# Optimization experiments

Measured on AMD Instinct MI355X. Metric: run time of the kernel, lower is better.

Reference implementation:

```python
import jax, jax.numpy as jnp
import numpy as np
import math

DIM = 2048
NUM_HEADS = 16
NUM_KV_HEADS = 4
HEAD_DIM = DIM // NUM_HEADS  # 128
KV_DIM = DIM * NUM_KV_HEADS // NUM_HEADS  # 512
B, T = 4, 2048


def setup_inputs() -> dict:
    key = jax.random.key(0)
    ks = jax.random.split(key, 12)
    s = 0.02
    return {
        "x": jax.random.normal(ks[0], (B, T, DIM), dtype=jnp.float32),
        "cos": jax.random.uniform(ks[1], (T, HEAD_DIM // 2), dtype=jnp.float32),
        "sin": jax.random.uniform(ks[2], (T, HEAD_DIM // 2), dtype=jnp.float32),
        "Wq": jax.random.normal(ks[3], (DIM, DIM), dtype=jnp.float32) * s,
        "bq": jnp.zeros((DIM,), dtype=jnp.float32),
        "Wk": jax.random.normal(ks[4], (DIM, KV_DIM), dtype=jnp.float32) * s,
        "bk": jnp.zeros((KV_DIM,), dtype=jnp.float32),
        "Wv": jax.random.normal(ks[5], (DIM, KV_DIM), dtype=jnp.float32) * s,
        "bv": jnp.zeros((KV_DIM,), dtype=jnp.float32),
        "Wo": jax.random.normal(ks[6], (DIM, DIM), dtype=jnp.float32) * s,
        "bo": jnp.zeros((DIM,), dtype=jnp.float32),
    }


def _rope(t, cos, sin):
    # t: [B, H, T, D]; cos/sin: [T, D/2] broadcast over (B, H)
    t1, t2 = t[..., ::2], t[..., 1::2]
    return jnp.concatenate([t1 * cos - t2 * sin, t1 * sin + t2 * cos], axis=-1)


def reference(x, cos, sin, Wq, bq, Wk, bk, Wv, bv, Wo, bo):
    Bx, Tx, C = x.shape
    q = (x @ Wq + bq).reshape(Bx, Tx, NUM_HEADS, HEAD_DIM).transpose(0, 2, 1, 3)
    k = (x @ Wk + bk).reshape(Bx, Tx, NUM_KV_HEADS, HEAD_DIM).transpose(0, 2, 1, 3)
    v = (x @ Wv + bv).reshape(Bx, Tx, NUM_KV_HEADS, HEAD_DIM).transpose(0, 2, 1, 3)
    rep = NUM_HEADS // NUM_KV_HEADS
    k = jnp.repeat(k, rep, axis=1)
    v = jnp.repeat(v, rep, axis=1)
    q = _rope(q, cos, sin)
    k = _rope(k, cos, sin)
    scores = jnp.einsum("bhqd,bhkd->bhqk", q, k) / math.sqrt(HEAD_DIM)
    attn = jax.nn.softmax(scores, axis=-1)
    out = jnp.einsum("bhqk,bhkd->bhqd", attn, v)
    out = out.transpose(0, 2, 1, 3).reshape(Bx, Tx, C)
    return out @ Wo + bo
```

## Files before the change

### kernel.cpp

```cpp
#include <hip/hip_runtime.h>

typedef unsigned short u16;
using bf16x8 = __attribute__((ext_vector_type(8))) short;
using u16x8  = __attribute__((ext_vector_type(8))) unsigned short;
using f32x4  = __attribute__((ext_vector_type(4))) float;
using f32x16 = __attribute__((ext_vector_type(16))) float;
using u32x4  = __attribute__((ext_vector_type(4))) unsigned int;

__device__ __forceinline__ u16 f2bf(float f) {
  unsigned u = __float_as_uint(f);
  u += 0x7FFFu + ((u >> 16) & 1u);
  return (u16)(u >> 16);
}

__device__ __forceinline__ unsigned cvt_pk_bf16(float lo, float hi) {
  unsigned r;
  asm("v_cvt_pk_bf16_f32 %0, %1, %2" : "=v"(r) : "v"(lo), "v"(hi));
  return r;
}

__device__ __forceinline__ void permswap(unsigned& a, unsigned& b) {
  asm volatile("v_permlane32_swap_b32 %0, %1" : "+v"(a), "+v"(b));
}

__device__ __forceinline__ void gload_lds16(const void* g, void* l) {
  __builtin_amdgcn_global_load_lds(
      (const __attribute__((address_space(1))) unsigned int*)g,
      (__attribute__((address_space(3))) unsigned int*)l, 16, 0, 0);
}

__global__ __launch_bounds__(256) void k_cvt(const float* __restrict__ src,
                                             u16* __restrict__ dst) {
  size_t i = (size_t)blockIdx.x * 256 + threadIdx.x;
  const float4* s4 = (const float4*)src;
  float4 a = s4[i * 2], b = s4[i * 2 + 1];
  u16x8 r;
  r[0] = f2bf(a.x); r[1] = f2bf(a.y); r[2] = f2bf(a.z); r[3] = f2bf(a.w);
  r[4] = f2bf(b.x); r[5] = f2bf(b.y); r[6] = f2bf(b.z); r[7] = f2bf(b.w);
  *(u16x8*)(dst + i * 8) = r;
}

__global__ void k_transpose_cvt(const float* __restrict__ src, u16* __restrict__ dst,
                                int R, int C) {
  __shared__ float tile[32][33];
  int bx = blockIdx.x * 32, by = blockIdx.y * 32;
  int tx = threadIdx.x, ty = threadIdx.y;
#pragma unroll
  for (int j = 0; j < 4; ++j)
    tile[ty + j * 8][tx] = src[(size_t)(by + ty + j * 8) * C + bx + tx];
  __syncthreads();
#pragma unroll
  for (int j = 0; j < 4; ++j)
    dst[(size_t)(bx + ty + j * 8) * R + by + tx] = f2bf(tile[tx][ty + j * 8]);
}

__device__ __forceinline__ void gemm_core128(const u16* __restrict__ A,
                                             const u16* __restrict__ Bt, int K,
                                             int m0, int n0, u16* As, u16* Bs,
                                             f32x4 acc[4][4]) {
  const int tid  = threadIdx.x;
  const int lane = tid & 63;
  const int w    = tid >> 6;
  const int wr   = (w >> 1) * 64;
  const int wc   = (w & 1) * 64;
  const int srow = (w << 3) + (lane >> 3);
  const int lm   = lane & 15;
  const int lg   = lane >> 4;

  for (int kt = 0; kt < K; kt += 64) {
#pragma unroll
    for (int i = 0; i < 4; ++i) {
      int r  = (i << 5) + srow;
      int cc = (lane & 7) ^ (r & 7);
      gload_lds16(A  + (size_t)(m0 + r) * K + kt + (cc << 3), As + ((i * 4 + w) << 9));
      gload_lds16(Bt + (size_t)(n0 + r) * K + kt + (cc << 3), Bs + ((i * 4 + w) << 9));
    }
    __syncthreads();
#pragma unroll
    for (int kk = 0; kk < 2; ++kk) {
      bf16x8 af[4], bfr[4];
#pragma unroll
      for (int m = 0; m < 4; ++m) {
        const int row = wr + m * 16 + lm;
        af[m] = *(const bf16x8*)(As + row * 64 + ((((kk << 2) + lg) ^ (row & 7)) << 3));
      }
#pragma unroll
      for (int n = 0; n < 4; ++n) {
        const int row = wc + n * 16 + lm;
        bfr[n] = *(const bf16x8*)(Bs + row * 64 + ((((kk << 2) + lg) ^ (row & 7)) << 3));
      }
#pragma unroll
      for (int m = 0; m < 4; ++m)
#pragma unroll
        for (int n = 0; n < 4; ++n)
          acc[m][n] = __builtin_amdgcn_mfma_f32_16x16x32_bf16(af[m], bfr[n], acc[m][n], 0, 0, 0);
    }
    __syncthreads();
  }
}

__global__ __launch_bounds__(256, 2) void k_qkv(
    const u16* __restrict__ xb, const u16* __restrict__ wT,
    const float* __restrict__ bq, const float* __restrict__ bk, const float* __restrict__ bv,
    const float* __restrict__ cosb, const float* __restrict__ sinb,
    u16* __restrict__ qbuf, u16* __restrict__ kbuf, u16* __restrict__ vbufT) {
  __shared__ u16 As[128 * 64], Bs[128 * 64];
  const int mt = blockIdx.x, nt = blockIdx.y;
  f32x4 acc[4][4];
#pragma unroll
  for (int m = 0; m < 4; ++m)
#pragma unroll
    for (int n = 0; n < 4; ++n) { f32x4 z = {0.f, 0.f, 0.f, 0.f}; acc[m][n] = z; }
  gemm_core128(xb, wT, 2048, mt * 128, nt * 128, As, Bs, acc);

  const int lane = threadIdx.x & 63, w = threadIdx.x >> 6;
  const int row0 = mt * 128 + (w >> 1) * 64 + ((lane >> 4) << 2);
  const int col0 = nt * 128 + (w & 1) * 64 + (lane & 15);
  const float qscale = 0.12751744f;

#pragma unroll
  for (int m = 0; m < 4; ++m) {
#pragma unroll
    for (int n = 0; n < 4; ++n) {
      const int gc = col0 + n * 16;
#pragma unroll
      for (int i = 0; i < 4; ++i) {
        const int gr = row0 + m * 16 + i;
        const int b = gr >> 11, t = gr & 2047;
        float v = acc[m][n][i];
        if (nt < 16) {
          int h = gc >> 7, d = gc & 127;
          float val = v + bq[gc];
          float part = __shfl_xor(val, 1);
          int ir = d >> 1;
          float c = cosb[t * 64 + ir], s = sinb[t * 64 + ir];
          float outv; int dd;
          if (d & 1) { outv = part * s + val * c; dd = ir + 64; }
          else       { outv = val * c - part * s; dd = ir; }
          qbuf[(((size_t)(b * 16 + h) * 2048 + t) << 7) + dd] = f2bf(outv * qscale);
        } else if (nt < 20) {
          int g2 = gc - 2048;
          int kvh = g2 >> 7, d = g2 & 127;
          float val = v + bk[g2];
          float part = __shfl_xor(val, 1);
          int ir = d >> 1;
          float c = cosb[t * 64 + ir], s = sinb[t * 64 + ir];
          float outv; int dd;
          if (d & 1) { outv = part * s + val * c; dd = ir + 64; }
          else       { outv = val * c - part * s; dd = ir; }
          kbuf[(((size_t)(b * 4 + kvh) * 2048 + t) << 7) + dd] = f2bf(outv);
        } else {
          int g2 = gc - 2560;
          int kvh = g2 >> 7, d = g2 & 127;
          float val = v + bv[g2];
          vbufT[((size_t)((b * 4 + kvh) * 128 + d)) * 2048 + t] = f2bf(val);
        }
      }
    }
  }
}

__global__ __launch_bounds__(256, 2) void k_attn(const u16* __restrict__ qbuf,
                                                 const u16* __restrict__ kbuf,
                                                 const u16* __restrict__ vbufT,
                                                 u16* __restrict__ ob) {
  __shared__ u16 Ks[2][64 * 128];
  __shared__ u16 Vs[2][128 * 64];

  const int f = blockIdx.x;
  const int x = f & 7, mm = f >> 3;
  const int g = x * 2 + (mm >> 6);
  const int mem = mm & 63;
  const int b = g >> 2, kvh = g & 3;
  const int h = kvh * 4 + (mem >> 4);
  const int qt = mem & 15;

  const int tid = threadIdx.x, lane = tid & 63, w = tid >> 6;
  const int l31 = lane & 31, hi = lane >> 5;

  const u16* qb = qbuf + ((size_t)((b * 16 + h) * 2048 + qt * 128)) * 128;
  const u16* kb = kbuf + ((size_t)(b * 4 + kvh) * 2048) * 128;
  const u16* vb = vbufT + ((size_t)(b * 4 + kvh) * 128) * 2048;

  const int q = w * 32 + l31;
  bf16x8 qfr[8];
#pragma unroll
  for (int kc = 0; kc < 8; ++kc)
    qfr[kc] = *(const bf16x8*)(qb + (size_t)q * 128 + kc * 16 + hi * 8);

  f32x16 o[4];
#pragma unroll
  for (int dt = 0; dt < 4; ++dt)
#pragma unroll
    for (int r = 0; r < 16; ++r) o[dt][r] = 0.f;
  float lsum = 0.f;

  auto stage = [&](int buf, int kt) {
#pragma unroll
    for (int j = 0; j < 4; ++j) {
      int s  = w * 4 + j;
      int cK = s * 64 + lane;
      int rK = cK >> 4, ccK = cK & 15;
      gload_lds16(kb + (size_t)(kt + rK) * 128 + ((ccK ^ (rK & 7)) << 3), &Ks[buf][s << 9]);
      int dV = s * 8 + (lane >> 3), ccV = lane & 7;
      gload_lds16(vb + (size_t)dV * 2048 + kt + ((ccV ^ (dV & 7)) << 3), &Vs[buf][s << 9]);
    }
  };

  stage(0, 0);
  for (int t = 0; t < 32; ++t) {
    if (t < 31) {
      stage((t + 1) & 1, (t + 1) << 6);
      asm volatile("s_waitcnt vmcnt(8)" ::: "memory");
    } else {
      asm volatile("s_waitcnt vmcnt(0)" ::: "memory");
    }
    __builtin_amdgcn_s_barrier();
    __builtin_amdgcn_sched_barrier(0);
    const u16* KsC = Ks[t & 1];
    const u16* VsC = Vs[t & 1];

    u32x4 pa[4];

#pragma unroll
    for (int kb2 = 0; kb2 < 2; ++kb2) {
      const int key = kb2 * 32 + l31;
      bf16x8 kf[8];
#pragma unroll
      for (int kc = 0; kc < 8; ++kc)
        kf[kc] = *(const bf16x8*)(KsC + key * 128 + (((kc * 2 + hi) ^ (key & 7)) << 3));
      f32x16 s;
#pragma unroll
      for (int r = 0; r < 16; ++r) s[r] = 0.f;
      __builtin_amdgcn_s_setprio(1);
#pragma unroll
      for (int kc = 0; kc < 8; ++kc)
        s = __builtin_amdgcn_mfma_f32_32x32x16_bf16(kf[kc], qfr[kc], s, 0, 0, 0);
      __builtin_amdgcn_s_setprio(0);

      unsigned c[8];
#pragma unroll
      for (int j = 0; j < 8; ++j) {
        float pa_ = __builtin_amdgcn_exp2f(s[2 * j]);
        float pb_ = __builtin_amdgcn_exp2f(s[2 * j + 1]);
        lsum += pa_ + pb_;
        c[j] = cvt_pk_bf16(pa_, pb_);
      }
      unsigned t0 = c[0], t1 = c[2]; permswap(t0, t1);
      unsigned t2 = c[1], t3 = c[3]; permswap(t2, t3);
      u32x4 f0; f0[0] = t0; f0[1] = t2; f0[2] = t1; f0[3] = t3;
      pa[kb2 * 2] = f0;
      unsigned t4 = c[4], t5 = c[6]; permswap(t4, t5);
      unsigned t6 = c[5], t7 = c[7]; permswap(t6, t7);
      u32x4 f1; f1[0] = t4; f1[1] = t6; f1[2] = t5; f1[3] = t7;
      pa[kb2 * 2 + 1] = f1;
    }

    __builtin_amdgcn_s_setprio(1);
#pragma unroll
    for (int dt = 0; dt < 4; ++dt) {
      const int d = dt * 32 + l31;
#pragma unroll
      for (int ks = 0; ks < 4; ++ks) {
        bf16x8 vf = *(const bf16x8*)(VsC + d * 64 + (((ks * 2 + hi) ^ (d & 7)) << 3));
        bf16x8 af = __builtin_bit_cast(bf16x8, pa[ks]);
        o[dt] = __builtin_amdgcn_mfma_f32_32x32x16_bf16(af, vf, o[dt], 0, 0, 0);
      }
    }
    __builtin_amdgcn_s_setprio(0);
    __builtin_amdgcn_sched_barrier(0);
    __builtin_amdgcn_s_barrier();
  }

  float L = lsum + __shfl_xor(lsum, 32);
  float invL = 1.0f / L;
  float iv[16];
#pragma unroll
  for (int r = 0; r < 16; ++r)
    iv[r] = __shfl(invL, (r & 3) + 8 * (r >> 2) + 4 * hi);
#pragma unroll
  for (int dt = 0; dt < 4; ++dt) {
    const int d = dt * 32 + l31;
#pragma unroll
    for (int r = 0; r < 16; ++r) {
      const int tq = qt * 128 + w * 32 + (r & 3) + 8 * (r >> 2) + 4 * hi;
      ob[((size_t)(b * 2048 + tq)) * 2048 + h * 128 + d] = f2bf(o[dt][r] * iv[r]);
    }
  }
}

__global__ __launch_bounds__(256, 2) void k_oproj(const u16* __restrict__ ab,
                                                  const u16* __restrict__ woT,
                                                  const float* __restrict__ bo,
                                                  float* __restrict__ out) {
  __shared__ u16 As[128 * 64], Bs[128 * 64];
  const int mt = blockIdx.x, nt = blockIdx.y;
  f32x4 acc[4][4];
#pragma unroll
  for (int m = 0; m < 4; ++m)
#pragma unroll
    for (int n = 0; n < 4; ++n) { f32x4 z = {0.f, 0.f, 0.f, 0.f}; acc[m][n] = z; }
  gemm_core128(ab, woT, 2048, mt * 128, nt * 128, As, Bs, acc);

  const int lane = threadIdx.x & 63, w = threadIdx.x >> 6;
  const int row0 = mt * 128 + (w >> 1) * 64 + ((lane >> 4) << 2);
  const int col0 = nt * 128 + (w & 1) * 64 + (lane & 15);
#pragma unroll
  for (int m = 0; m < 4; ++m)
#pragma unroll
    for (int n = 0; n < 4; ++n) {
      const int gc = col0 + n * 16;
      const float bias = bo[gc];
#pragma unroll
      for (int i = 0; i < 4; ++i) {
        const int gr = row0 + m * 16 + i;
        out[(size_t)gr * 2048 + gc] = acc[m][n][i] + bias;
      }
    }
}

extern "C" void kernel_launch(void* const* d_in, const int* in_sizes, int n_in,
                              void* d_out, int out_size, void* d_ws, size_t ws_size,
                              hipStream_t stream) {
  const float* x    = (const float*)d_in[0];
  const float* cosb = (const float*)d_in[1];
  const float* sinb = (const float*)d_in[2];
  const float* Wq   = (const float*)d_in[3];
  const float* bq   = (const float*)d_in[4];
  const float* Wk   = (const float*)d_in[5];
  const float* bk   = (const float*)d_in[6];
  const float* Wv   = (const float*)d_in[7];
  const float* bv   = (const float*)d_in[8];
  const float* Wo   = (const float*)d_in[9];
  const float* bo   = (const float*)d_in[10];
  float* out = (float*)d_out;

  u16* ws    = (u16*)d_ws;
  u16* xb    = ws;
  u16* wqkvT = xb    + (size_t)8192 * 2048;
  u16* woT   = wqkvT + (size_t)3072 * 2048;
  u16* qbuf  = woT   + (size_t)2048 * 2048;
  u16* kbuf  = qbuf  + (size_t)8192 * 2048;
  u16* vbufT = kbuf  + (size_t)8192 * 512;
  u16* attn  = xb;

  k_cvt<<<8192, 256, 0, stream>>>(x, xb);
  dim3 tb(32, 8);
  k_transpose_cvt<<<dim3(64, 64), tb, 0, stream>>>(Wq, wqkvT, 2048, 2048);
  k_transpose_cvt<<<dim3(16, 64), tb, 0, stream>>>(Wk, wqkvT + (size_t)2048 * 2048, 2048, 512);
  k_transpose_cvt<<<dim3(16, 64), tb, 0, stream>>>(Wv, wqkvT + (size_t)2560 * 2048, 2048, 512);
  k_transpose_cvt<<<dim3(64, 64), tb, 0, stream>>>(Wo, woT, 2048, 2048);

  k_qkv<<<dim3(64, 24), 256, 0, stream>>>(xb, wqkvT, bq, bk, bv, cosb, sinb, qbuf, kbuf, vbufT);
  k_attn<<<1024, 256, 0, stream>>>(qbuf, kbuf, vbufT, attn);
  k_oproj<<<dim3(64, 16), 256, 0, stream>>>(attn, woT, bo, out);
}
```

Baseline: 368.5 us.

## Single-buffer V tile in attention, loading it during the QK^T phase

Changes the V shared-memory tile from double-buffered to single-buffered. Each V tile is now issued at the start of its own iteration, so its load overlaps the QK^T MFMAs and softmax, and an extra waitcnt plus barrier sits before the PV stage. This cuts LDS use by 16KB per block, which could allow more resident blocks. The cost is less lookahead for V loads and one more barrier per iteration.

```diff
diff --git a/kernel.cpp b/kernel.cpp
--- a/kernel.cpp
+++ b/kernel.cpp
@@ -165,7 +165,7 @@
                                                  const u16* __restrict__ vbufT,
                                                  u16* __restrict__ ob) {
   __shared__ u16 Ks[2][64 * 128];
-  __shared__ u16 Vs[2][128 * 64];
+  __shared__ u16 Vs[128 * 64];
 
   const int f = blockIdx.x;
   const int x = f & 7, mm = f >> 3;
@@ -195,30 +195,35 @@
     for (int r = 0; r < 16; ++r) o[dt][r] = 0.f;
   float lsum = 0.f;
 
-  auto stage = [&](int buf, int kt) {
+  auto stageK = [&](int buf, int kt) {
 #pragma unroll
     for (int j = 0; j < 4; ++j) {
       int s  = w * 4 + j;
       int cK = s * 64 + lane;
       int rK = cK >> 4, ccK = cK & 15;
       gload_lds16(kb + (size_t)(kt + rK) * 128 + ((ccK ^ (rK & 7)) << 3), &Ks[buf][s << 9]);
+    }
+  };
+  auto stageV = [&](int kt) {
+#pragma unroll
+    for (int j = 0; j < 4; ++j) {
+      int s  = w * 4 + j;
       int dV = s * 8 + (lane >> 3), ccV = lane & 7;
-      gload_lds16(vb + (size_t)dV * 2048 + kt + ((ccV ^ (dV & 7)) << 3), &Vs[buf][s << 9]);
+      gload_lds16(vb + (size_t)dV * 2048 + kt + ((ccV ^ (dV & 7)) << 3), &Vs[s << 9]);
     }
   };
 
-  stage(0, 0);
+  stageK(0, 0);
   for (int t = 0; t < 32; ++t) {
-    if (t < 31) {
-      stage((t + 1) & 1, (t + 1) << 6);
-      asm volatile("s_waitcnt vmcnt(8)" ::: "memory");
-    } else {
-      asm volatile("s_waitcnt vmcnt(0)" ::: "memory");
-    }
+    const int kt = t << 6;
+    if (t < 31) stageK((t + 1) & 1, kt + 64);
+    stageV(kt);
+
+    if (t < 31) { asm volatile("s_waitcnt vmcnt(8)" ::: "memory"); }
+    else        { asm volatile("s_waitcnt vmcnt(4)" ::: "memory"); }
     __builtin_amdgcn_s_barrier();
     __builtin_amdgcn_sched_barrier(0);
     const u16* KsC = Ks[t & 1];
-    const u16* VsC = Vs[t & 1];
 
     u32x4 pa[4];
 
@@ -256,13 +261,18 @@
       pa[kb2 * 2 + 1] = f1;
     }
 
+    if (t < 31) { asm volatile("s_waitcnt vmcnt(4)" ::: "memory"); }
+    else        { asm volatile("s_waitcnt vmcnt(0)" ::: "memory"); }
+    __builtin_amdgcn_s_barrier();
+    __builtin_amdgcn_sched_barrier(0);
+
     __builtin_amdgcn_s_setprio(1);
 #pragma unroll
     for (int dt = 0; dt < 4; ++dt) {
       const int d = dt * 32 + l31;
 #pragma unroll
       for (int ks = 0; ks < 4; ++ks) {
-        bf16x8 vf = *(const bf16x8*)(VsC + d * 64 + (((ks * 2 + hi) ^ (d & 7)) << 3));
+        bf16x8 vf = *(const bf16x8*)(Vs + d * 64 + (((ks * 2 + hi) ^ (d & 7)) << 3));
         bf16x8 af = __builtin_bit_cast(bf16x8, pa[ks]);
         o[dt] = __builtin_amdgcn_mfma_f32_32x32x16_bf16(af, vf, o[dt], 0, 0, 0);
       }
```

Result: no change. 371.9 us (+0.9%).
